# Kernel tuning notes

Hardware: AMD Instinct MI355X
Metric: run time of the kernel (lower is better)

## Reference

```python
import jax, jax.numpy as jnp
import numpy as np

DIM = 1024
NUM_HEADS = 16
HEAD_DIM = DIM // NUM_HEADS
SCALE = HEAD_DIM ** -0.25
EPS = 1e-5


def layer_norm(x, w, b):
    mu = jnp.mean(x, axis=-1, keepdims=True)
    var = jnp.var(x, axis=-1, keepdims=True)
    return (x - mu) * jax.lax.rsqrt(var + EPS) * w + b


def setup_inputs() -> dict:
    key = jax.random.key(0)
    ks = jax.random.split(key, 10)
    b, l, d = 2, 2048, DIM
    x = jax.random.normal(ks[0], (b, l, d), dtype=jnp.float32)
    # causal mask, broadcastable over heads: [b, 1, l, l]
    causal = jnp.tril(jnp.ones((l, l), dtype=jnp.int32))
    mask = jnp.broadcast_to(causal[None, None], (b, 1, l, l))
    s = 0.02
    return {
        "x": x,
        "mask": mask,
        "ln1_w": jnp.ones((d,), jnp.float32),
        "ln1_b": jnp.zeros((d,), jnp.float32),
        "qkv_w": jax.random.normal(ks[1], (d, 3 * d), jnp.float32) * s,
        "qkv_b": jnp.zeros((3 * d,), jnp.float32),
        "proj_w": jax.random.normal(ks[2], (d, d), jnp.float32) * s,
        "proj_b": jnp.zeros((d,), jnp.float32),
        "ln2_w": jnp.ones((d,), jnp.float32),
        "ln2_b": jnp.zeros((d,), jnp.float32),
        "ffn_w1": jax.random.normal(ks[3], (d, 4 * d), jnp.float32) * s,
        "ffn_b1": jnp.zeros((4 * d,), jnp.float32),
        "ffn_w2": jax.random.normal(ks[4], (4 * d, d), jnp.float32) * s,
        "ffn_b2": jnp.zeros((d,), jnp.float32),
    }


def attention(x, mask, qkv_w, qkv_b, proj_w, proj_b):
    b, l, d = x.shape
    n, c = NUM_HEADS, HEAD_DIM
    qkv = (x @ qkv_w + qkv_b).reshape(b, l, n * 3, c)
    q, k, v = qkv[:, :, :n], qkv[:, :, n:2 * n], qkv[:, :, 2 * n:]
    # scores: [b, n, l, l], scale applied to both q and k (head_dim^-0.25 each)
    attn = jnp.einsum('binc,bjnc->bnij', q * SCALE, k * SCALE)
    attn = jnp.where(mask[:, :, :l, :l] == 0, -jnp.inf, attn)
    attn = jax.nn.softmax(attn.astype(jnp.float32), axis=-1).astype(x.dtype)
    out = jnp.einsum('bnij,bjnc->binc', attn, v).reshape(b, l, d)
    return out @ proj_w + proj_b


def reference(x, mask, ln1_w, ln1_b, qkv_w, qkv_b, proj_w, proj_b,
              ln2_w, ln2_b, ffn_w1, ffn_b1, ffn_w2, ffn_b2):
    h = x + attention(layer_norm(x, ln1_w, ln1_b), mask, qkv_w, qkv_b, proj_w, proj_b)
    y = layer_norm(h, ln2_w, ln2_b)
    ffn = jax.nn.gelu(y @ ffn_w1 + ffn_b1, approximate=False) @ ffn_w2 + ffn_b2
    return h + ffn
```

## Files before the change

kernel.cpp:

```cpp
#include <hip/hip_runtime.h>
#include <hip/hip_bf16.h>
#include <math.h>

typedef __attribute__((ext_vector_type(8))) short bf16x8;
typedef __attribute__((ext_vector_type(4))) float f32x4;
typedef __attribute__((ext_vector_type(4))) unsigned u32x4;

#define MFMA16(a, b, c) __builtin_amdgcn_mfma_f32_16x16x32_bf16((a), (b), (c), 0, 0, 0)

typedef const __attribute__((address_space(1))) void* gas_ptr;
typedef __attribute__((address_space(3))) void* las_ptr;

__device__ __forceinline__ unsigned pack_bf16(float a, float b) {
    unsigned ua = (unsigned)__bfloat16_as_ushort(__float2bfloat16(a));
    unsigned ub = (unsigned)__bfloat16_as_ushort(__float2bfloat16(b));
    return ua | (ub << 16);
}

__global__ __launch_bounds__(256)
void transpose_to_bf16(const float* __restrict__ in, __hip_bfloat16* __restrict__ out,
                       int K, int N)
{
    __shared__ float t[32][33];
    const int tx = threadIdx.x & 31, ty = threadIdx.x >> 5;
    const int n0 = blockIdx.x * 32, k0 = blockIdx.y * 32;
    #pragma unroll
    for (int j = 0; j < 32; j += 8)
        t[ty + j][tx] = in[(size_t)(k0 + ty + j) * N + n0 + tx];
    __syncthreads();
    #pragma unroll
    for (int j = 0; j < 32; j += 8)
        out[(size_t)(n0 + ty + j) * K + k0 + tx] = __float2bfloat16(t[tx][ty + j]);
}

__global__ __launch_bounds__(256)
void ln_kernel(const float* __restrict__ in, const float* __restrict__ w,
               const float* __restrict__ b, __hip_bfloat16* __restrict__ out)
{
    const int row = blockIdx.x;
    const int tid = threadIdx.x;
    const float4 v = reinterpret_cast<const float4*>(in + (size_t)row * 1024)[tid];
    float s  = v.x + v.y + v.z + v.w;
    float s2 = v.x * v.x + v.y * v.y + v.z * v.z + v.w * v.w;
    #pragma unroll
    for (int off = 32; off > 0; off >>= 1) {
        s  += __shfl_down(s,  off);
        s2 += __shfl_down(s2, off);
    }
    __shared__ float red[8];
    const int wv = tid >> 6, ln = tid & 63;
    if (ln == 0) { red[wv] = s; red[4 + wv] = s2; }
    __syncthreads();
    s  = red[0] + red[1] + red[2] + red[3];
    s2 = red[4] + red[5] + red[6] + red[7];
    const float mu   = s * (1.0f / 1024.0f);
    const float var  = s2 * (1.0f / 1024.0f) - mu * mu;
    const float rstd = rsqrtf(var + 1e-5f);
    const float4 wv4 = reinterpret_cast<const float4*>(w)[tid];
    const float4 bv4 = reinterpret_cast<const float4*>(b)[tid];
    const size_t o = (size_t)row * 1024 + tid * 4;
    out[o + 0] = __float2bfloat16((v.x - mu) * rstd * wv4.x + bv4.x);
    out[o + 1] = __float2bfloat16((v.y - mu) * rstd * wv4.y + bv4.y);
    out[o + 2] = __float2bfloat16((v.z - mu) * rstd * wv4.z + bv4.z);
    out[o + 3] = __float2bfloat16((v.w - mu) * rstd * wv4.w + bv4.w);
}

template<int MODE>
__global__ __launch_bounds__(256, 3)
void gemm128p(const __hip_bfloat16* __restrict__ A,
              const __hip_bfloat16* __restrict__ Bt,
              const float* __restrict__ bias,
              const float* __restrict__ resid,
              void* __restrict__ C0, void* __restrict__ C1,
              int N, int K)
{
    constexpr int SLOT = 8192;
    __shared__ __align__(16) __hip_bfloat16 lds[3 * SLOT];

    const int tid  = threadIdx.x;
    const int lane = tid & 63;
    const int w    = tid >> 6;
    const int wr   = w >> 1, wc = w & 1;
    const int fr   = lane & 15, fq = lane >> 4;

    const int gx  = gridDim.x;
    const int nsq = (gx * gridDim.y) >> 4;
    const int ngx = gx >> 2;
    const int flat = blockIdx.y * gx + blockIdx.x;
    const int idx  = flat >> 3;
    const int sq   = (flat & 7) * (nsq >> 3) + (idx >> 4);
    const int pos  = idx & 15;
    const int bx = (sq % ngx) * 4 + (pos & 3);
    const int by = (sq / ngx) * 4 + (pos >> 2);
    const int m0 = by * 128, n0 = bx * 128;
    const int NT = K >> 5;

    const int prc = w * 8 + (lane >> 3);
    const int ch  = lane & 7;
    const __hip_bfloat16* aS[2];
    const __hip_bfloat16* bS[2];
    #pragma unroll
    for (int j = 0; j < 2; ++j) {
        const int pr  = prc + 32 * j;
        const int v   = ch ^ (pr & 7);
        const int row = 2 * pr + (v >> 2);
        const int col = 8 * (v & 3);
        aS[j] = A  + (size_t)(m0 + row) * K + col;
        bS[j] = Bt + (size_t)(n0 + row) * K + col;
    }

    auto stage = [&](int kt, int s) {
        __hip_bfloat16* LA = &lds[s * SLOT];
        __hip_bfloat16* LB = LA + 4096;
        #pragma unroll
        for (int j = 0; j < 2; ++j) {
            __builtin_amdgcn_global_load_lds((gas_ptr)(const void*)(aS[j] + kt * 32),
                                             (las_ptr)(void*)(LA + w * 512 + j * 2048), 16, 0, 0);
            __builtin_amdgcn_global_load_lds((gas_ptr)(const void*)(bS[j] + kt * 32),
                                             (las_ptr)(void*)(LB + w * 512 + j * 2048), 16, 0, 0);
        }
    };

    f32x4 acc[4][4] = {};

    stage(0, 0);
    stage(1, 1);
    int sl = 0, sp = 2;

    for (int kt = 0; kt < NT; ++kt) {
        if (kt + 1 < NT)
            asm volatile("s_waitcnt vmcnt(4) lgkmcnt(0)" ::: "memory");
        else
            asm volatile("s_waitcnt vmcnt(0) lgkmcnt(0)" ::: "memory");
        __builtin_amdgcn_s_barrier();
        __builtin_amdgcn_sched_barrier(0);

        if (kt + 2 < NT) stage(kt + 2, sp);

        const __hip_bfloat16* LA = &lds[sl * SLOT];
        const __hip_bfloat16* LB = LA + 4096;
        bf16x8 af[4], bg[4];
        #pragma unroll
        for (int m = 0; m < 4; ++m) {
            const int r = wr * 64 + m * 16 + fr;
            af[m] = *reinterpret_cast<const bf16x8*>(
                &LA[(r >> 1) * 64 + (((r & 1) * 32 + fq * 8) ^ (((r >> 1) & 7) * 8))]);
        }
        #pragma unroll
        for (int n = 0; n < 4; ++n) {
            const int r = wc * 64 + n * 16 + fr;
            bg[n] = *reinterpret_cast<const bf16x8*>(
                &LB[(r >> 1) * 64 + (((r & 1) * 32 + fq * 8) ^ (((r >> 1) & 7) * 8))]);
        }

        __builtin_amdgcn_s_setprio(1);
        #pragma unroll
        for (int m = 0; m < 4; ++m)
            #pragma unroll
            for (int n = 0; n < 4; ++n)
                acc[m][n] = MFMA16(af[m], bg[n], acc[m][n]);
        __builtin_amdgcn_s_setprio(0);

        sl = (sl == 2) ? 0 : sl + 1;
        sp = (sp == 2) ? 0 : sp + 1;
    }

    if (MODE == 3 && n0 >= 2048) {
        #pragma unroll
        for (int n = 0; n < 4; ++n) {
            const int col = n0 + wc * 64 + n * 16 + fr;
            const int hc  = col - 2048;
            const float bv = bias[col];
            #pragma unroll
            for (int m = 0; m < 4; ++m) {
                const int r0 = m0 + wr * 64 + m * 16 + fq * 4;
                const int b = r0 >> 11, l0 = r0 & 2047;
                const unsigned lo = pack_bf16(acc[m][n][0] + bv, acc[m][n][1] + bv);
                const unsigned hi = pack_bf16(acc[m][n][2] + bv, acc[m][n][3] + bv);
                uint2 pv; pv.x = lo; pv.y = hi;
                *reinterpret_cast<uint2*>(
                    &reinterpret_cast<__hip_bfloat16*>(C1)[((size_t)(b * 1024 + hc) << 11) + l0]) = pv;
            }
        }
        return;
    }

    #pragma unroll
    for (int n = 0; n < 4; ++n) {
        const int col = n0 + wc * 64 + n * 16 + fr;
        const float bv = bias[col];
        #pragma unroll
        for (int m = 0; m < 4; ++m) {
            #pragma unroll
            for (int i = 0; i < 4; ++i) {
                const int row = m0 + wr * 64 + m * 16 + fq * 4 + i;
                float v = acc[m][n][i] + bv;
                if (MODE == 2) {
                    v = 0.5f * v * (1.0f + erff(v * 0.70710678118654752f));
                    reinterpret_cast<__hip_bfloat16*>(C0)[(size_t)row * N + col] =
                        __float2bfloat16(v);
                } else if (MODE == 3) {
                    reinterpret_cast<__hip_bfloat16*>(C0)[((size_t)row << 11) + col] =
                        __float2bfloat16(v);
                } else {
                    v += resid[(size_t)row * N + col];
                    reinterpret_cast<float*>(C0)[(size_t)row * N + col] = v;
                }
            }
        }
    }
}

__global__ __launch_bounds__(256)
void attn_kernel(const __hip_bfloat16* __restrict__ qk,
                 const __hip_bfloat16* __restrict__ Vt,
                 __hip_bfloat16* __restrict__ out)
{
    const int bid  = blockIdx.x;
    const int xcd  = bid & 7;
    const int rank = bid >> 3;
    const int panel = xcd * 4 + (rank & 3);
    const int qt   = 31 - (rank >> 2);
    const int h = panel & 15, b = panel >> 4;
    const int q0 = qt * 64;

    const int lane = threadIdx.x & 63;
    const int w    = threadIdx.x >> 6;
    const int fr   = lane & 15, fq = lane >> 4;
    const int qrow = q0 + w * 16 + fr;

    __shared__ __align__(16) __hip_bfloat16 Klds[2][64 * 64];
    __shared__ __align__(16) __hip_bfloat16 Vlds[2][64 * 64];

    bf16x8 qf[2];
    {
        const __hip_bfloat16* qp = qk + ((size_t)(b * 2048 + qrow) << 11) + h * 64 + fq * 8;
        qf[0] = *reinterpret_cast<const bf16x8*>(qp);
        qf[1] = *reinterpret_cast<const bf16x8*>(qp + 32);
    }

    const int srow8 = lane >> 3;
    const int sc    = lane & 7;
    const __hip_bfloat16* Kg[2];
    const __hip_bfloat16* Vg[2];
    #pragma unroll
    for (int j = 0; j < 2; ++j) {
        const int r = w * 16 + j * 8 + srow8;
        const int csw = (sc ^ (r & 7)) * 8;
        Kg[j] = qk + ((size_t)(b * 2048 + r) << 11) + 1024 + h * 64 + csw;
        Vg[j] = Vt + ((size_t)(b * 1024 + h * 64 + r) << 11) + csw;
    }

    auto stage = [&](int kv0, int bufi) {
        __hip_bfloat16* KL = &Klds[bufi][0];
        __hip_bfloat16* VL = &Vlds[bufi][0];
        #pragma unroll
        for (int j = 0; j < 2; ++j) {
            __builtin_amdgcn_global_load_lds(
                (gas_ptr)(const void*)(Kg[j] + ((size_t)kv0 << 11)),
                (las_ptr)(void*)&KL[(w * 16 + j * 8) * 64], 16, 0, 0);
            __builtin_amdgcn_global_load_lds(
                (gas_ptr)(const void*)(Vg[j] + kv0),
                (las_ptr)(void*)&VL[(w * 16 + j * 8) * 64], 16, 0, 0);
        }
    };

    const float SC = 0.125f * 1.44269504088896f;
    float m_run = -1e30f, l_run = 0.0f;
    f32x4 o[4] = {};

    const int ntiles = qt + 1;
    stage(0, 0);
    int cur = 0;

    for (int t = 0; t < ntiles; ++t) {
        const int kv0 = t << 6;
        __syncthreads();
        if (t + 1 < ntiles) stage((t + 1) << 6, cur ^ 1);

        const __hip_bfloat16* Kl = &Klds[cur][0];
        const __hip_bfloat16* Vl = &Vlds[cur][0];

        f32x4 s[4] = {};
        #pragma unroll
        for (int n = 0; n < 4; ++n) {
            const int row = n * 16 + fr;
            const int sw = (row & 7) << 3;
            const bf16x8 k0 = *reinterpret_cast<const bf16x8*>(&Kl[row * 64 + ((fq * 8) ^ sw)]);
            const bf16x8 k1 = *reinterpret_cast<const bf16x8*>(&Kl[row * 64 + ((fq * 8 + 32) ^ sw)]);
            s[n] = MFMA16(k0, qf[0], s[n]);
            s[n] = MFMA16(k1, qf[1], s[n]);
        }

        float pm = -1e30f;
        if (t == ntiles - 1) {
            #pragma unroll
            for (int n = 0; n < 4; ++n)
                #pragma unroll
                for (int i = 0; i < 4; ++i) {
                    const int kvp = kv0 + n * 16 + fq * 4 + i;
                    float sv = s[n][i] * SC;
                    sv = (kvp <= qrow) ? sv : -1e30f;
                    s[n][i] = sv;
                    pm = fmaxf(pm, sv);
                }
        } else {
            #pragma unroll
            for (int n = 0; n < 4; ++n)
                #pragma unroll
                for (int i = 0; i < 4; ++i) {
                    const float sv = s[n][i] * SC;
                    s[n][i] = sv;
                    pm = fmaxf(pm, sv);
                }
        }
        pm = fmaxf(pm, __shfl_xor(pm, 16));
        pm = fmaxf(pm, __shfl_xor(pm, 32));
        const float mnew = fmaxf(m_run, pm);
        const float corr = exp2f(m_run - mnew);
        m_run = mnew;

        float rs = 0.0f;
        unsigned pk[8];
        #pragma unroll
        for (int n = 0; n < 4; ++n) {
            const float p0 = exp2f(s[n][0] - mnew);
            const float p1 = exp2f(s[n][1] - mnew);
            const float p2 = exp2f(s[n][2] - mnew);
            const float p3 = exp2f(s[n][3] - mnew);
            rs += (p0 + p1) + (p2 + p3);
            pk[n * 2 + 0] = pack_bf16(p0, p1);
            pk[n * 2 + 1] = pack_bf16(p2, p3);
        }
        rs += __shfl_xor(rs, 16);
        rs += __shfl_xor(rs, 32);
        l_run = l_run * corr + rs;

        #pragma unroll
        for (int i = 0; i < 4; ++i) {
            const float ci = __shfl(corr, fq * 4 + i);
            o[0][i] *= ci; o[1][i] *= ci; o[2][i] *= ci; o[3][i] *= ci;
        }

        u32x4 A0, A1;
        #pragma unroll
        for (int r = 0; r < 4; ++r) {
            const int sl = fr + ((2 * (fq & 1) + (r >> 1)) << 4);
            const unsigned lo0 = __shfl(pk[0 + (r & 1)], sl);
            const unsigned hi0 = __shfl(pk[2 + (r & 1)], sl);
            const unsigned lo1 = __shfl(pk[4 + (r & 1)], sl);
            const unsigned hi1 = __shfl(pk[6 + (r & 1)], sl);
            A0[r] = (fq & 2) ? hi0 : lo0;
            A1[r] = (fq & 2) ? hi1 : lo1;
        }
        const bf16x8 pa0 = __builtin_bit_cast(bf16x8, A0);
        const bf16x8 pa1 = __builtin_bit_cast(bf16x8, A1);

        #pragma unroll
        for (int tt = 0; tt < 4; ++tt) {
            const int row = tt * 16 + fr;
            const int sw = (row & 7) << 3;
            const bf16x8 v0 = *reinterpret_cast<const bf16x8*>(&Vl[row * 64 + ((fq * 8) ^ sw)]);
            const bf16x8 v1 = *reinterpret_cast<const bf16x8*>(&Vl[row * 64 + ((fq * 8 + 32) ^ sw)]);
            o[tt] = MFMA16(pa0, v0, o[tt]);
            o[tt] = MFMA16(pa1, v1, o[tt]);
        }
        cur ^= 1;
    }

    #pragma unroll
    for (int i = 0; i < 4; ++i) {
        const float li  = __shfl(l_run, fq * 4 + i);
        const float inv = 1.0f / li;
        const int row = q0 + w * 16 + fq * 4 + i;
        #pragma unroll
        for (int tt = 0; tt < 4; ++tt)
            out[(size_t)(b * 2048 + row) * 1024 + h * 64 + tt * 16 + fr] =
                __float2bfloat16(o[tt][i] * inv);
    }
}

extern "C" void kernel_launch(void* const* d_in, const int* in_sizes, int n_in,
                              void* d_out, int out_size, void* d_ws, size_t ws_size,
                              hipStream_t stream)
{
    (void)in_sizes; (void)n_in; (void)out_size; (void)ws_size;
    const float* x      = (const float*)d_in[0];
    const float* ln1_w  = (const float*)d_in[2];
    const float* ln1_b  = (const float*)d_in[3];
    const float* qkv_w  = (const float*)d_in[4];
    const float* qkv_b  = (const float*)d_in[5];
    const float* proj_w = (const float*)d_in[6];
    const float* proj_b = (const float*)d_in[7];
    const float* ln2_w  = (const float*)d_in[8];
    const float* ln2_b  = (const float*)d_in[9];
    const float* ffn_w1 = (const float*)d_in[10];
    const float* ffn_b1 = (const float*)d_in[11];
    const float* ffn_w2 = (const float*)d_in[12];
    const float* ffn_b2 = (const float*)d_in[13];
    float* outp = (float*)d_out;

    char* ws = (char*)d_ws;
    size_t off = 0;
    auto take = [&](size_t bytes) -> char* {
        char* p = ws + off;
        off += (bytes + 255) & ~(size_t)255;
        return p;
    };
    __hip_bfloat16* wqkv  = (__hip_bfloat16*)take((size_t)3072 * 1024 * 2);
    __hip_bfloat16* wproj = (__hip_bfloat16*)take((size_t)1024 * 1024 * 2);
    __hip_bfloat16* wff1  = (__hip_bfloat16*)take((size_t)4096 * 1024 * 2);
    __hip_bfloat16* wff2  = (__hip_bfloat16*)take((size_t)1024 * 4096 * 2);
    float*          hbuf  = (float*)take((size_t)4096 * 1024 * 4);
    __hip_bfloat16* xn    = (__hip_bfloat16*)take((size_t)4096 * 1024 * 2);
    __hip_bfloat16* qkb   = (__hip_bfloat16*)take((size_t)4096 * 2048 * 2);
    __hip_bfloat16* Vt    = (__hip_bfloat16*)take((size_t)2048 * 2048 * 2);
    __hip_bfloat16* attn  = (__hip_bfloat16*)take((size_t)4096 * 1024 * 2);
    __hip_bfloat16* ffn1  = qkb;

    transpose_to_bf16<<<dim3(3072 / 32, 1024 / 32), 256, 0, stream>>>(qkv_w, wqkv, 1024, 3072);
    transpose_to_bf16<<<dim3(1024 / 32, 1024 / 32), 256, 0, stream>>>(proj_w, wproj, 1024, 1024);
    transpose_to_bf16<<<dim3(4096 / 32, 1024 / 32), 256, 0, stream>>>(ffn_w1, wff1, 1024, 4096);
    transpose_to_bf16<<<dim3(1024 / 32, 4096 / 32), 256, 0, stream>>>(ffn_w2, wff2, 4096, 1024);

    ln_kernel<<<4096, 256, 0, stream>>>(x, ln1_w, ln1_b, xn);
    gemm128p<3><<<dim3(24, 32), 256, 0, stream>>>(
        xn, wqkv, qkv_b, nullptr, qkb, Vt, 3072, 1024);
    attn_kernel<<<1024, 256, 0, stream>>>(qkb, Vt, attn);
    gemm128p<0><<<dim3(8, 32), 256, 0, stream>>>(
        attn, wproj, proj_b, x, hbuf, nullptr, 1024, 1024);
    ln_kernel<<<4096, 256, 0, stream>>>(hbuf, ln2_w, ln2_b, xn);
    gemm128p<2><<<dim3(32, 32), 256, 0, stream>>>(
        xn, wff1, ffn_b1, nullptr, ffn1, nullptr, 4096, 1024);
    gemm128p<0><<<dim3(8, 32), 256, 0, stream>>>(
        ffn1, wff2, ffn_b2, hbuf, outp, nullptr, 1024, 4096);
}
```

Before: 242.9 us.

## Add 256x256-tile GEMM with split-K for FFN2 and a reduce kernel

Adds a 512-thread GEMM kernel with 256x256 output tiles and a 4-stage LDS pipeline that loads A and B through global_load_lds. Each K-step issues its loads and MFMAs in two halves to raise data reuse per tile. This kernel replaces the 128x128 GEMM for the QKV, FFN1 and FFN2 matmuls. FFN2 is split along K into two partial outputs, and a new elementwise kernel adds the partials, the bias and the residual. The larger tiles cut global and LDS traffic per FLOP, but the grids shrink to 128–256 workgroups, which can underfill the CUs. Split-K also adds an extra 16MB fp32 partial buffer (aliased onto the weight workspace) plus the reduce pass.

```diff
diff --git a/kernel.cpp b/kernel.cpp
--- a/kernel.cpp
+++ b/kernel.cpp
@@ -65,13 +65,12 @@
     out[o + 3] = __float2bfloat16((v.w - mu) * rstd * wv4.w + bv4.w);
 }
 
-template<int MODE>
 __global__ __launch_bounds__(256, 3)
 void gemm128p(const __hip_bfloat16* __restrict__ A,
               const __hip_bfloat16* __restrict__ Bt,
               const float* __restrict__ bias,
               const float* __restrict__ resid,
-              void* __restrict__ C0, void* __restrict__ C1,
+              float* __restrict__ C0,
               int N, int K)
 {
     constexpr int SLOT = 8192;
@@ -83,15 +82,10 @@
     const int wr   = w >> 1, wc = w & 1;
     const int fr   = lane & 15, fq = lane >> 4;
 
-    const int gx  = gridDim.x;
-    const int nsq = (gx * gridDim.y) >> 4;
-    const int ngx = gx >> 2;
-    const int flat = blockIdx.y * gx + blockIdx.x;
-    const int idx  = flat >> 3;
-    const int sq   = (flat & 7) * (nsq >> 3) + (idx >> 4);
-    const int pos  = idx & 15;
-    const int bx = (sq % ngx) * 4 + (pos & 3);
-    const int by = (sq / ngx) * 4 + (pos >> 2);
+    const int nwg = gridDim.x * gridDim.y;
+    int flat = blockIdx.y * gridDim.x + blockIdx.x;
+    flat = (flat & 7) * (nwg >> 3) + (flat >> 3);
+    const int bx = flat % gridDim.x, by = flat / gridDim.x;
     const int m0 = by * 128, n0 = bx * 128;
     const int NT = K >> 5;
 
@@ -165,19 +159,150 @@
         sp = (sp == 2) ? 0 : sp + 1;
     }
 
+    #pragma unroll
+    for (int n = 0; n < 4; ++n) {
+        const int col = n0 + wc * 64 + n * 16 + fr;
+        const float bv = bias[col];
+        #pragma unroll
+        for (int m = 0; m < 4; ++m)
+            #pragma unroll
+            for (int i = 0; i < 4; ++i) {
+                const int row = m0 + wr * 64 + m * 16 + fq * 4 + i;
+                C0[(size_t)row * N + col] = acc[m][n][i] + bv + resid[(size_t)row * N + col];
+            }
+    }
+}
+
+template<int MODE>
+__global__ __launch_bounds__(512, 1)
+void gemm256p(const __hip_bfloat16* __restrict__ A,
+              const __hip_bfloat16* __restrict__ Bt,
+              const float* __restrict__ bias,
+              void* __restrict__ C0, void* __restrict__ C1,
+              int N, int K, int KS)
+{
+    constexpr int SLOT = 16384;
+    __shared__ __align__(16) __hip_bfloat16 lds[4 * SLOT];
+
+    const int tid  = threadIdx.x;
+    const int lane = tid & 63;
+    const int w    = tid >> 6;
+    const int wm   = w >> 2, wn = w & 3;
+    const int fr   = lane & 15, fq = lane >> 4;
+
+    const int nwg = gridDim.x * gridDim.y;
+    int flat = blockIdx.y * gridDim.x + blockIdx.x;
+    flat = (flat & 7) * (nwg >> 3) + (flat >> 3);
+    const int bx = flat % gridDim.x, by = flat / gridDim.x;
+    const int m0 = by * 256, n0 = bx * 256;
+    const int kbase = blockIdx.z * KS;
+    const int NT = KS >> 5;
+
+    const __hip_bfloat16* aS[2];
+    const __hip_bfloat16* bS[2];
+    #pragma unroll
+    for (int j = 0; j < 2; ++j) {
+        const int c   = tid + 512 * j;
+        const int row = c >> 2;
+        const int lc  = (c & 3) ^ ((row >> 1) & 3);
+        aS[j] = A  + (size_t)(m0 + row) * K + kbase + lc * 8;
+        bS[j] = Bt + (size_t)(n0 + row) * K + kbase + lc * 8;
+    }
+
+    auto stageA = [&](int kt) {
+        __hip_bfloat16* L = &lds[(kt & 3) * SLOT];
+        #pragma unroll
+        for (int j = 0; j < 2; ++j)
+            __builtin_amdgcn_global_load_lds((gas_ptr)(const void*)(aS[j] + kt * 32),
+                                             (las_ptr)(void*)(L + w * 512 + j * 4096), 16, 0, 0);
+    };
+    auto stageB = [&](int kt) {
+        __hip_bfloat16* L = &lds[(kt & 3) * SLOT] + 8192;
+        #pragma unroll
+        for (int j = 0; j < 2; ++j)
+            __builtin_amdgcn_global_load_lds((gas_ptr)(const void*)(bS[j] + kt * 32),
+                                             (las_ptr)(void*)(L + w * 512 + j * 4096), 16, 0, 0);
+    };
+
+    f32x4 acc[8][4] = {};
+
+    stageA(0); stageB(0);
+    stageA(1); stageB(1);
+    stageA(2); stageB(2);
+    asm volatile("s_waitcnt vmcnt(8)" ::: "memory");
+    __builtin_amdgcn_s_barrier();
+    __builtin_amdgcn_sched_barrier(0);
+
+    for (int kt = 0; kt < NT; ++kt) {
+        const __hip_bfloat16* LA = &lds[(kt & 3) * SLOT];
+        const __hip_bfloat16* LB = LA + 8192;
+        bf16x8 af[4], bg[4];
+
+        #pragma unroll
+        for (int m = 0; m < 4; ++m) {
+            const int r = wm * 128 + m * 16 + fr;
+            af[m] = *reinterpret_cast<const bf16x8*>(
+                &LA[r * 32 + ((fq ^ ((r >> 1) & 3)) << 3)]);
+        }
+        #pragma unroll
+        for (int n = 0; n < 4; ++n) {
+            const int r = wn * 64 + n * 16 + fr;
+            bg[n] = *reinterpret_cast<const bf16x8*>(
+                &LB[r * 32 + ((fq ^ ((r >> 1) & 3)) << 3)]);
+        }
+        if (kt + 3 < NT) stageA(kt + 3);
+        __builtin_amdgcn_sched_barrier(0);
+        __builtin_amdgcn_s_barrier();
+        asm volatile("s_waitcnt lgkmcnt(0)" ::: "memory");
+        __builtin_amdgcn_sched_barrier(0);
+        __builtin_amdgcn_s_setprio(1);
+        #pragma unroll
+        for (int m = 0; m < 4; ++m)
+            #pragma unroll
+            for (int n = 0; n < 4; ++n)
+                acc[m][n] = MFMA16(af[m], bg[n], acc[m][n]);
+        __builtin_amdgcn_s_setprio(0);
+        __builtin_amdgcn_sched_barrier(0);
+        __builtin_amdgcn_s_barrier();
+
+        #pragma unroll
+        for (int m = 0; m < 4; ++m) {
+            const int r = wm * 128 + 64 + m * 16 + fr;
+            af[m] = *reinterpret_cast<const bf16x8*>(
+                &LA[r * 32 + ((fq ^ ((r >> 1) & 3)) << 3)]);
+        }
+        if (kt + 3 < NT) stageB(kt + 3);
+        __builtin_amdgcn_sched_barrier(0);
+        __builtin_amdgcn_s_barrier();
+        asm volatile("s_waitcnt lgkmcnt(0)" ::: "memory");
+        __builtin_amdgcn_sched_barrier(0);
+        __builtin_amdgcn_s_setprio(1);
+        #pragma unroll
+        for (int m = 0; m < 4; ++m)
+            #pragma unroll
+            for (int n = 0; n < 4; ++n)
+                acc[4 + m][n] = MFMA16(af[m], bg[n], acc[4 + m][n]);
+        __builtin_amdgcn_s_setprio(0);
+        __builtin_amdgcn_sched_barrier(0);
+        if (kt + 3 < NT)      asm volatile("s_waitcnt vmcnt(8)" ::: "memory");
+        else if (kt + 2 < NT) asm volatile("s_waitcnt vmcnt(4)" ::: "memory");
+        else                  asm volatile("s_waitcnt vmcnt(0)" ::: "memory");
+        __builtin_amdgcn_s_barrier();
+    }
+
     if (MODE == 3 && n0 >= 2048) {
         #pragma unroll
         for (int n = 0; n < 4; ++n) {
-            const int col = n0 + wc * 64 + n * 16 + fr;
+            const int col = n0 + wn * 64 + n * 16 + fr;
             const int hc  = col - 2048;
             const float bv = bias[col];
             #pragma unroll
-            for (int m = 0; m < 4; ++m) {
-                const int r0 = m0 + wr * 64 + m * 16 + fq * 4;
+            for (int a = 0; a < 8; ++a) {
+                const int r0 = m0 + wm * 128 + (a >> 2) * 64 + (a & 3) * 16 + fq * 4;
                 const int b = r0 >> 11, l0 = r0 & 2047;
-                const unsigned lo = pack_bf16(acc[m][n][0] + bv, acc[m][n][1] + bv);
-                const unsigned hi = pack_bf16(acc[m][n][2] + bv, acc[m][n][3] + bv);
-                uint2 pv; pv.x = lo; pv.y = hi;
+                uint2 pv;
+                pv.x = pack_bf16(acc[a][n][0] + bv, acc[a][n][1] + bv);
+                pv.y = pack_bf16(acc[a][n][2] + bv, acc[a][n][3] + bv);
                 *reinterpret_cast<uint2*>(
                     &reinterpret_cast<__hip_bfloat16*>(C1)[((size_t)(b * 1024 + hc) << 11) + l0]) = pv;
             }
@@ -187,14 +312,15 @@
 
     #pragma unroll
     for (int n = 0; n < 4; ++n) {
-        const int col = n0 + wc * 64 + n * 16 + fr;
-        const float bv = bias[col];
-        #pragma unroll
-        for (int m = 0; m < 4; ++m) {
+        const int col = n0 + wn * 64 + n * 16 + fr;
+        float bv = 0.0f;
+        if (MODE != 4) bv = bias[col];
+        #pragma unroll
+        for (int a = 0; a < 8; ++a) {
             #pragma unroll
             for (int i = 0; i < 4; ++i) {
-                const int row = m0 + wr * 64 + m * 16 + fq * 4 + i;
-                float v = acc[m][n][i] + bv;
+                const int row = m0 + wm * 128 + (a >> 2) * 64 + (a & 3) * 16 + fq * 4 + i;
+                float v = acc[a][n][i] + bv;
                 if (MODE == 2) {
                     v = 0.5f * v * (1.0f + erff(v * 0.70710678118654752f));
                     reinterpret_cast<__hip_bfloat16*>(C0)[(size_t)row * N + col] =
@@ -203,12 +329,27 @@
                     reinterpret_cast<__hip_bfloat16*>(C0)[((size_t)row << 11) + col] =
                         __float2bfloat16(v);
                 } else {
-                    v += resid[(size_t)row * N + col];
-                    reinterpret_cast<float*>(C0)[(size_t)row * N + col] = v;
+                    float* dst = blockIdx.z ? reinterpret_cast<float*>(C1)
+                                            : reinterpret_cast<float*>(C0);
+                    dst[(size_t)row * N + col] = v;
                 }
             }
         }
     }
+}
+
+__global__ __launch_bounds__(256)
+void ffn2_reduce(const float4* __restrict__ p0, float4* __restrict__ outv,
+                 const float4* __restrict__ h, const float4* __restrict__ bias)
+{
+    const int i = blockIdx.x * 256 + threadIdx.x;
+    const float4 a = p0[i], b = outv[i], c = h[i], d = bias[i & 255];
+    float4 r;
+    r.x = a.x + b.x + c.x + d.x;
+    r.y = a.y + b.y + c.y + d.y;
+    r.z = a.z + b.z + c.z + d.z;
+    r.w = a.w + b.w + c.w + d.w;
+    outv[i] = r;
 }
 
 __global__ __launch_bounds__(256)
@@ -417,6 +558,7 @@
     __hip_bfloat16* Vt    = (__hip_bfloat16*)take((size_t)2048 * 2048 * 2);
     __hip_bfloat16* attn  = (__hip_bfloat16*)take((size_t)4096 * 1024 * 2);
     __hip_bfloat16* ffn1  = qkb;
+    float* part0 = (float*)ws;
 
     transpose_to_bf16<<<dim3(3072 / 32, 1024 / 32), 256, 0, stream>>>(qkv_w, wqkv, 1024, 3072);
     transpose_to_bf16<<<dim3(1024 / 32, 1024 / 32), 256, 0, stream>>>(proj_w, wproj, 1024, 1024);
@@ -424,14 +566,16 @@
     transpose_to_bf16<<<dim3(1024 / 32, 4096 / 32), 256, 0, stream>>>(ffn_w2, wff2, 4096, 1024);
 
     ln_kernel<<<4096, 256, 0, stream>>>(x, ln1_w, ln1_b, xn);
-    gemm128p<3><<<dim3(24, 32), 256, 0, stream>>>(
-        xn, wqkv, qkv_b, nullptr, qkb, Vt, 3072, 1024);
+    gemm256p<3><<<dim3(12, 16, 1), 512, 0, stream>>>(
+        xn, wqkv, qkv_b, qkb, Vt, 3072, 1024, 1024);
     attn_kernel<<<1024, 256, 0, stream>>>(qkb, Vt, attn);
-    gemm128p<0><<<dim3(8, 32), 256, 0, stream>>>(
-        attn, wproj, proj_b, x, hbuf, nullptr, 1024, 1024);
+    gemm128p<<<dim3(8, 32), 256, 0, stream>>>(
+        attn, wproj, proj_b, x, hbuf, 1024, 1024);
     ln_kernel<<<4096, 256, 0, stream>>>(hbuf, ln2_w, ln2_b, xn);
-    gemm128p<2><<<dim3(32, 32), 256, 0, stream>>>(
-        xn, wff1, ffn_b1, nullptr, ffn1, nullptr, 4096, 1024);
-    gemm128p<0><<<dim3(8, 32), 256, 0, stream>>>(
-        ffn1, wff2, ffn_b2, hbuf, outp, nullptr, 1024, 4096);
-}
+    gemm256p<2><<<dim3(16, 16, 1), 512, 0, stream>>>(
+        xn, wff1, ffn_b1, ffn1, nullptr, 4096, 1024, 1024);
+    gemm256p<4><<<dim3(4, 16, 2), 512, 0, stream>>>(
+        ffn1, wff2, nullptr, part0, outp, 1024, 4096, 2048);
+    ffn2_reduce<<<4096, 256, 0, stream>>>(
+        (const float4*)part0, (float4*)outp, (const float4*)hbuf, (const float4*)ffn_b2);
+}
```

After: 268.4 us. 1.1x slower.

## Stage GEMM epilogue through LDS for coalesced 16-byte bf16 stores

Applied to the files above, without the earlier changes.

The bf16-output GEMM modes now write the bias-added (and GELU'd) tile into swizzled LDS, then read it back in row-major or transposed order so each thread emits 16-byte vector stores. This replaces the scattered 2-byte and 8-byte global writes in the epilogue, including the transposed V output. The tile-to-workgroup mapping is also simplified from a 4x4 supertile swizzle to a plain XCD-round-robin remap, which can change L2 locality. The staging costs extra LDS traffic and two barriers per tile.

```diff
diff --git a/kernel.cpp b/kernel.cpp
--- a/kernel.cpp
+++ b/kernel.cpp
@@ -83,15 +83,10 @@
     const int wr   = w >> 1, wc = w & 1;
     const int fr   = lane & 15, fq = lane >> 4;
 
-    const int gx  = gridDim.x;
-    const int nsq = (gx * gridDim.y) >> 4;
-    const int ngx = gx >> 2;
-    const int flat = blockIdx.y * gx + blockIdx.x;
-    const int idx  = flat >> 3;
-    const int sq   = (flat & 7) * (nsq >> 3) + (idx >> 4);
-    const int pos  = idx & 15;
-    const int bx = (sq % ngx) * 4 + (pos & 3);
-    const int by = (sq / ngx) * 4 + (pos >> 2);
+    const int nwg = gridDim.x * gridDim.y;
+    int flat = blockIdx.y * gridDim.x + blockIdx.x;
+    flat = (flat & 7) * (nwg >> 3) + (flat >> 3);
+    const int bx = flat % gridDim.x, by = flat / gridDim.x;
     const int m0 = by * 128, n0 = bx * 128;
     const int NT = K >> 5;
 
@@ -165,49 +160,78 @@
         sp = (sp == 2) ? 0 : sp + 1;
     }
 
-    if (MODE == 3 && n0 >= 2048) {
+    if (MODE == 0) {
         #pragma unroll
         for (int n = 0; n < 4; ++n) {
             const int col = n0 + wc * 64 + n * 16 + fr;
-            const int hc  = col - 2048;
             const float bv = bias[col];
             #pragma unroll
-            for (int m = 0; m < 4; ++m) {
-                const int r0 = m0 + wr * 64 + m * 16 + fq * 4;
-                const int b = r0 >> 11, l0 = r0 & 2047;
-                const unsigned lo = pack_bf16(acc[m][n][0] + bv, acc[m][n][1] + bv);
-                const unsigned hi = pack_bf16(acc[m][n][2] + bv, acc[m][n][3] + bv);
-                uint2 pv; pv.x = lo; pv.y = hi;
-                *reinterpret_cast<uint2*>(
-                    &reinterpret_cast<__hip_bfloat16*>(C1)[((size_t)(b * 1024 + hc) << 11) + l0]) = pv;
+            for (int m = 0; m < 4; ++m)
+                #pragma unroll
+                for (int i = 0; i < 4; ++i) {
+                    const int row = m0 + wr * 64 + m * 16 + fq * 4 + i;
+                    reinterpret_cast<float*>(C0)[(size_t)row * N + col] =
+                        acc[m][n][i] + bv + resid[(size_t)row * N + col];
+                }
+        }
+        return;
+    }
+
+    __syncthreads();
+    ushort* E = reinterpret_cast<ushort*>(lds);
+    auto eaddr = [](int r, int c16) { return r * 128 + (((c16) ^ ((r >> 3) & 15)) << 3); };
+
+    #pragma unroll
+    for (int n = 0; n < 4; ++n) {
+        const int col = wc * 64 + n * 16 + fr;
+        const float bv = bias[n0 + col];
+        #pragma unroll
+        for (int m = 0; m < 4; ++m) {
+            #pragma unroll
+            for (int i = 0; i < 4; ++i) {
+                const int row = wr * 64 + m * 16 + fq * 4 + i;
+                float v = acc[m][n][i] + bv;
+                if (MODE == 2) v = 0.5f * v * (1.0f + erff(v * 0.70710678118654752f));
+                E[eaddr(row, col >> 3) + (col & 7)] =
+                    __bfloat16_as_ushort(__float2bfloat16(v));
             }
         }
+    }
+    __syncthreads();
+
+    if (MODE == 3 && n0 >= 2048) {
+        const int bq    = m0 >> 11;
+        const int lbase = m0 & 2047;
+        const int hcb   = n0 - 2048;
+        #pragma unroll
+        for (int p = 0; p < 8; ++p) {
+            const int id  = p * 256 + tid;
+            const int hcl = id >> 4;
+            const int lc  = id & 15;
+            u32x4 pkt;
+            #pragma unroll
+            for (int k2 = 0; k2 < 4; ++k2) {
+                const int l0 = lc * 8 + k2 * 2;
+                const unsigned a = E[eaddr(l0,     hcl >> 3) + (hcl & 7)];
+                const unsigned b = E[eaddr(l0 + 1, hcl >> 3) + (hcl & 7)];
+                pkt[k2] = a | (b << 16);
+            }
+            *reinterpret_cast<u32x4*>(
+                &reinterpret_cast<__hip_bfloat16*>(C1)
+                    [((size_t)(bq * 1024 + hcb + hcl) << 11) + lbase + lc * 8]) = pkt;
+        }
         return;
     }
 
-    #pragma unroll
-    for (int n = 0; n < 4; ++n) {
-        const int col = n0 + wc * 64 + n * 16 + fr;
-        const float bv = bias[col];
-        #pragma unroll
-        for (int m = 0; m < 4; ++m) {
-            #pragma unroll
-            for (int i = 0; i < 4; ++i) {
-                const int row = m0 + wr * 64 + m * 16 + fq * 4 + i;
-                float v = acc[m][n][i] + bv;
-                if (MODE == 2) {
-                    v = 0.5f * v * (1.0f + erff(v * 0.70710678118654752f));
-                    reinterpret_cast<__hip_bfloat16*>(C0)[(size_t)row * N + col] =
-                        __float2bfloat16(v);
-                } else if (MODE == 3) {
-                    reinterpret_cast<__hip_bfloat16*>(C0)[((size_t)row << 11) + col] =
-                        __float2bfloat16(v);
-                } else {
-                    v += resid[(size_t)row * N + col];
-                    reinterpret_cast<float*>(C0)[(size_t)row * N + col] = v;
-                }
-            }
-        }
+    const size_t ldC = (MODE == 3) ? 2048 : (size_t)N;
+    __hip_bfloat16* Cb = reinterpret_cast<__hip_bfloat16*>(C0);
+    #pragma unroll
+    for (int p = 0; p < 8; ++p) {
+        const int id  = p * 256 + tid;
+        const int row = id >> 4;
+        const int c16 = id & 15;
+        const bf16x8 vv = *reinterpret_cast<const bf16x8*>(&E[eaddr(row, c16)]);
+        *reinterpret_cast<bf16x8*>(&Cb[(size_t)(m0 + row) * ldC + n0 + c16 * 8]) = vv;
     }
 }
 
@@ -345,11 +369,11 @@
         u32x4 A0, A1;
         #pragma unroll
         for (int r = 0; r < 4; ++r) {
-            const int sl = fr + ((2 * (fq & 1) + (r >> 1)) << 4);
-            const unsigned lo0 = __shfl(pk[0 + (r & 1)], sl);
-            const unsigned hi0 = __shfl(pk[2 + (r & 1)], sl);
-            const unsigned lo1 = __shfl(pk[4 + (r & 1)], sl);
-            const unsigned hi1 = __shfl(pk[6 + (r & 1)], sl);
+            const int slx = fr + ((2 * (fq & 1) + (r >> 1)) << 4);
+            const unsigned lo0 = __shfl(pk[0 + (r & 1)], slx);
+            const unsigned hi0 = __shfl(pk[2 + (r & 1)], slx);
+            const unsigned lo1 = __shfl(pk[4 + (r & 1)], slx);
+            const unsigned hi1 = __shfl(pk[6 + (r & 1)], slx);
             A0[r] = (fq & 2) ? hi0 : lo0;
             A1[r] = (fq & 2) ? hi1 : lo1;
         }
```

Measured after the change: 246.4 us. About the same (+1.4%).
